# Kernel optimization log

Measured on AMD Instinct MI355X. Metric: run time of the kernel, lower is better.

Reference implementation:

```python
import jax, jax.numpy as jnp
import numpy as np


def setup_inputs() -> dict:
    key = jax.random.key(0)
    ks = jax.random.split(key, 16)
    B, S, D, H = 32, 2048, 512, 512
    s = 1.0 / np.sqrt(H)
    inp = {
        "x": jax.random.normal(ks[0], (B, H), jnp.float32),
        "context": jax.random.normal(ks[1], (B, S, D), jnp.float32),
        "mask": jnp.zeros((B, S), jnp.bool_),  # False = valid position
        "Wi": jax.random.normal(ks[2], (H, H), jnp.float32) * s,
        "bi": jax.random.normal(ks[3], (H,), jnp.float32) * s,
        "Wc0": jax.random.normal(ks[4], (H, D), jnp.float32) * s,
        "bc0": jax.random.normal(ks[5], (H,), jnp.float32) * s,
        "Wc1": jax.random.normal(ks[6], (H, D), jnp.float32) * s,
        "bc1": jax.random.normal(ks[7], (H,), jnp.float32) * s,
        "Wc2": jax.random.normal(ks[8], (H, D), jnp.float32) * s,
        "bc2": jax.random.normal(ks[9], (H,), jnp.float32) * s,
        "Wc3": jax.random.normal(ks[10], (H, D), jnp.float32) * s,
        "bc3": jax.random.normal(ks[11], (H,), jnp.float32) * s,
        "V": jax.random.uniform(ks[12], (H,), jnp.float32, -s, s),
    }
    return inp


def reference(x, context, mask, Wi, bi, Wc0, bc0, Wc1, bc1, Wc2, bc2, Wc3, bc3, V):
    # mask: True = masked out in the original API; module flips it first.
    valid = ~mask  # [B, S], True = keep

    inp = (x @ Wi.T + bi)[:, :, None]  # [B, H, 1]

    def proj(W, b):
        # Conv1d(D, H, kernel=1) on context.permute(0,2,1) == token-wise GEMM
        return jnp.einsum("bsd,hd->bhs", context, W) + b[None, :, None]  # [B, H, S]

    ctx = jnp.concatenate(
        [proj(Wc0, bc0), proj(Wc1, bc1), proj(Wc2, bc2), proj(Wc3, bc3)], axis=2
    )  # [B, H, 4S]

    t = jnp.tanh(inp + ctx)                      # [B, H, 4S]
    att = jnp.einsum("h,bhs->bs", V, t)          # bmm(V[B,1,H], t).squeeze(1)
    att = 10.0 * jnp.tanh(att)                   # [B, 4S]

    valid4 = jnp.tile(valid, (1, 4))             # mask.repeat(1, 4)
    att = jnp.where(valid4, att, -jnp.inf)
    # torch.no_grad() around the masked fill detaches the rest of the graph
    att = jax.lax.stop_gradient(att)

    ans = jax.nn.softmax(att, axis=1)            # [B, 4S]
    p = jnp.max(ans, axis=1)
    indices = jnp.argmax(ans, axis=1)
    return indices[:, None], p[:, None], mask
```

## Files before the change

### kernel.cpp

```cpp
#include <hip/hip_runtime.h>
#include <math.h>

typedef __bf16 bf16x8 __attribute__((ext_vector_type(8)));
typedef float f32x4 __attribute__((ext_vector_type(4)));
typedef short short8v __attribute__((ext_vector_type(8)));

#define MARGIN 0.01f
#define NCAND 32

#define WAITL  do { asm volatile("s_waitcnt lgkmcnt(0)" ::: "memory"); __builtin_amdgcn_sched_barrier(0); } while (0)
#define WAITV0 do { asm volatile("s_waitcnt vmcnt(0)" ::: "memory"); __builtin_amdgcn_sched_barrier(0); } while (0)
#define WAITV3 do { asm volatile("s_waitcnt vmcnt(3)" ::: "memory"); __builtin_amdgcn_sched_barrier(0); } while (0)
#define BARR   do { __builtin_amdgcn_s_barrier(); __builtin_amdgcn_sched_barrier(0); } while (0)

__device__ __forceinline__ unsigned short f2bf(float f) {
  unsigned u = __float_as_uint(f);
  u += 0x7fffu + ((u >> 16) & 1u);
  return (unsigned short)(u >> 16);
}
__device__ __forceinline__ float tanh_fast(float x) {
  float e = __builtin_amdgcn_exp2f(x * 2.885390081777927f);
  return 1.f - 2.f * __builtin_amdgcn_rcpf(e + 1.f);
}
__device__ __forceinline__ void gl_lds16(const void* g, void* l) {
  __builtin_amdgcn_global_load_lds(
      (const __attribute__((address_space(1))) unsigned int*)g,
      (__attribute__((address_space(3))) unsigned int*)l, 16, 0, 0);
}
__device__ __forceinline__ int cvt_pk_bf16(float lo, float hi) {
  int r;
  asm("v_cvt_pk_bf16_f32 %0, %1, %2" : "=v"(r) : "v"(lo), "v"(hi));
  return r;
}
__device__ __forceinline__ float dpp_row_reduce(float v) {
  int x;
  x = __builtin_amdgcn_update_dpp(0, __builtin_bit_cast(int, v), 0x118, 0xf, 0xf, true);
  v += __builtin_bit_cast(float, x);
  x = __builtin_amdgcn_update_dpp(0, __builtin_bit_cast(int, v), 0x114, 0xf, 0xf, true);
  v += __builtin_bit_cast(float, x);
  x = __builtin_amdgcn_update_dpp(0, __builtin_bit_cast(int, v), 0x112, 0xf, 0xf, true);
  v += __builtin_bit_cast(float, x);
  x = __builtin_amdgcn_update_dpp(0, __builtin_bit_cast(int, v), 0x111, 0xf, 0xf, true);
  v += __builtin_bit_cast(float, x);
  return v;
}

__global__ __launch_bounds__(256) void prep_small_k(
    const float* __restrict__ x, const float* __restrict__ Wi,
    const float* __restrict__ bi,
    const float* __restrict__ w0, const float* __restrict__ w1,
    const float* __restrict__ w2, const float* __restrict__ w3,
    short* __restrict__ Whi, float* __restrict__ inp) {
  int bid = blockIdx.x;
  if (bid < 512) {
    int gid = bid * 256 + threadIdx.x;
    int c = gid & 3, row = (gid >> 2) & 511, TK = gid >> 11;
    int TN = TK >> 4, KS = TK & 15;
    const float* w = (TN == 0) ? w0 : (TN == 1) ? w1 : (TN == 2) ? w2 : w3;
    const float* src = w + (size_t)row * 512 + KS * 32 + c * 8;
    float f[8];
    *(float4*)&f[0] = *(const float4*)(src);
    *(float4*)&f[4] = *(const float4*)(src + 4);
    short8v hv;
    #pragma unroll
    for (int i = 0; i < 8; ++i) hv[i] = (short)f2bf(f[i]);
    *(short8v*)(Whi + (size_t)gid * 8) = hv;
  } else {
    int gid = (bid - 512) * 256 + threadIdx.x;
    int b = gid >> 9, h = gid & 511;
    const float* xr = x + b * 512;
    const float* wr = Wi + h * 512;
    float acc = bi[h];
    #pragma unroll 4
    for (int k = 0; k < 512; k += 4) {
      float4 xv = *(const float4*)(xr + k);
      float4 wv = *(const float4*)(wr + k);
      acc += xv.x * wv.x + xv.y * wv.y + xv.z * wv.z + xv.w * wv.w;
    }
    inp[gid] = acc;
  }
}

__global__ __launch_bounds__(1024, 4) void gemm_att_k(
    const float* __restrict__ ctx, const short* __restrict__ Whi,
    const float* __restrict__ inp,
    const float* __restrict__ bc0, const float* __restrict__ bc1,
    const float* __restrict__ bc2, const float* __restrict__ bc3,
    const float* __restrict__ V, float* __restrict__ att) {
  __shared__ __align__(16) char smem[3][49152];

  const int t = threadIdx.x;
  int d = blockIdx.x + (blockIdx.y << 3);
  int work = (d & 7) * 256 + (d >> 3);
  int mt = work >> 2, nt = work & 3;
  int b = mt >> 4;
  const float* bc = (nt == 0) ? bc0 : (nt == 1) ? bc1 : (nt == 2) ? bc2 : bc3;

  const int ar = t >> 3, apos = t & 7;
  const int aq = apos ^ (ar & 7);
  const float* aSrc = ctx + ((size_t)mt * 128 + ar) * 512 + aq * 4;

  auto stageA = [&](int tile, int slot) {
    gl_lds16(aSrc + tile * 32, (float*)&smem[slot][0] + t * 4);
  };
  auto stageB = [&](int tile, int slot) {
    const short* gB = Whi + (((size_t)nt * 16 + tile) << 14) + t * 8;
    short* lB = (short*)&smem[slot][16384] + t * 8;
    gl_lds16(gB,        lB);
    gl_lds16(gB + 8192, lB + 8192);
  };

  f32x4 acc[4][4];
  #pragma unroll
  for (int i = 0; i < 4; ++i)
    #pragma unroll
    for (int j = 0; j < 4; ++j) acc[i][j] = (f32x4){0.f, 0.f, 0.f, 0.f};

  const int lane = t & 63, wid = t >> 6;
  const int wr = wid >> 3, wc = wid & 7;
  const int fr = lane & 15, fq = lane >> 4;
  const int s7 = fr & 7;
  const int p0 = (fq * 2) ^ s7;
  const int bbase = (wc * 64 + fr) * 32 + fq * 8;

  stageA(0, 0); stageB(0, 0);
  stageA(1, 1); stageB(1, 1);
  WAITV3;
  BARR;

  #pragma unroll
  for (int tt = 0; tt < 16; ++tt) {
    const int slot = tt % 3;
    const float* As = (const float*)&smem[slot][0];
    const short* Bs = (const short*)&smem[slot][16384];
    if (tt < 14) { stageA(tt + 2, (tt + 2) % 3); stageB(tt + 2, (tt + 2) % 3); }
    bf16x8 a[4], bv[4];
    #pragma unroll
    for (int mi = 0; mi < 4; ++mi) {
      int rowb = (wr * 64 + mi * 16 + fr) * 32;
      f32x4 c0 = *(const f32x4*)(As + rowb + p0 * 4);
      f32x4 c1 = *(const f32x4*)(As + rowb + (p0 ^ 1) * 4);
      int4 w;
      w.x = cvt_pk_bf16(c0[0], c0[1]);
      w.y = cvt_pk_bf16(c0[2], c0[3]);
      w.z = cvt_pk_bf16(c1[0], c1[1]);
      w.w = cvt_pk_bf16(c1[2], c1[3]);
      a[mi] = __builtin_bit_cast(bf16x8, w);
    }
    #pragma unroll
    for (int ni = 0; ni < 4; ++ni) bv[ni] = *(const bf16x8*)(Bs + bbase + ni * 512);
    WAITL;
    __builtin_amdgcn_s_setprio(1);
    #pragma unroll
    for (int mi = 0; mi < 4; ++mi)
      #pragma unroll
      for (int ni = 0; ni < 4; ++ni)
        acc[mi][ni] = __builtin_amdgcn_mfma_f32_16x16x32_bf16(a[mi], bv[ni], acc[mi][ni], 0, 0, 0);
    __builtin_amdgcn_s_setprio(0);
    __builtin_amdgcn_sched_barrier(0);
    if (tt < 14) { WAITV3; }
    else if (tt == 14) { WAITV0; }
    BARR;
  }

  float vV[4], vP[4];
  #pragma unroll
  for (int ni = 0; ni < 4; ++ni) {
    int j = wc * 64 + ni * 16 + fr;
    vV[ni] = V[j];
    vP[ni] = inp[b * 512 + j] + bc[j];
  }
  size_t abatt = (size_t)b * 8192 + (size_t)nt * 2048;
  #pragma unroll
  for (int mi = 0; mi < 4; ++mi) {
    #pragma unroll
    for (int r = 0; r < 4; ++r) {
      float sum = 0.f;
      #pragma unroll
      for (int ni = 0; ni < 4; ++ni)
        sum += vV[ni] * tanh_fast(vP[ni] + acc[mi][ni][r]);
      sum = dpp_row_reduce(sum);
      if (fr == 15) {
        int s2 = (mt & 15) * 128 + wr * 64 + mi * 16 + fq * 4 + r;
        atomicAdd(&att[abatt + s2], sum);
      }
    }
  }
}

__global__ __launch_bounds__(1024) void tail_k(const float* __restrict__ att,
    const unsigned char* __restrict__ mask, const float* __restrict__ ctx,
    const float* __restrict__ Wc0, const float* __restrict__ Wc1,
    const float* __restrict__ Wc2, const float* __restrict__ Wc3,
    const float* __restrict__ bc0, const float* __restrict__ bc1,
    const float* __restrict__ bc2, const float* __restrict__ bc3,
    const float* __restrict__ inp, const float* __restrict__ V,
    float* __restrict__ out) {
  int b = blockIdx.x, t = threadIdx.x;
  __shared__ float sred[1024];
  __shared__ float sctx[512];
  __shared__ int scnt;
  __shared__ int scand_j[NCAND];
  __shared__ float scand_a[NCAND];
  __shared__ float sexact[NCAND];

  if (t == 0) scnt = 0;
  float bm = -1e30f;
  for (int j = t; j < 8192; j += 1024) {
    if (mask[b * 2048 + (j & 2047)]) continue;
    bm = fmaxf(bm, att[(size_t)b * 8192 + j]);
  }
  sred[t] = bm;
  __syncthreads();
  for (int s2 = 512; s2 > 0; s2 >>= 1) {
    if (t < s2) sred[t] = fmaxf(sred[t], sred[t + s2]);
    __syncthreads();
  }
  float mx = sred[0];
  float Lref = 10.f * tanhf(mx);
  __syncthreads();
  float se = 0.f;
  for (int j = t; j < 8192; j += 1024) {
    if (mask[b * 2048 + (j & 2047)]) continue;
    float a = att[(size_t)b * 8192 + j];
    se += expf(10.f * tanhf(a) - Lref);
    if (a >= mx - MARGIN) {
      int slot = atomicAdd(&scnt, 1);
      if (slot < NCAND) { scand_j[slot] = j; scand_a[slot] = a; }
    }
  }
  sred[t] = se;
  __syncthreads();
  for (int s2 = 512; s2 > 0; s2 >>= 1) {
    if (t < s2) sred[t] += sred[t + s2];
    __syncthreads();
  }
  float den = sred[0];
  int n = min(scnt, NCAND);
  for (int j = t; j < 2048; j += 1024)
    out[64 + b * 2048 + j] = mask[b * 2048 + j] ? 1.0f : 0.0f;
  for (int i = 0; i < n; ++i) {
    int jj = scand_j[i];
    int g = jj >> 11, s = jj & 2047;
    const float* W  = (g == 0) ? Wc0 : (g == 1) ? Wc1 : (g == 2) ? Wc2 : Wc3;
    const float* bc = (g == 0) ? bc0 : (g == 1) ? bc1 : (g == 2) ? bc2 : bc3;
    const float* cr = ctx + ((size_t)b * 2048 + s) * 512;
    __syncthreads();
    if (t < 512) sctx[t] = cr[t];
    __syncthreads();
    float total = 0.f;
    if (t < 512) {
      const float* wrp = W + (size_t)t * 512;
      float acc = 0.f;
      #pragma unroll 4
      for (int k = 0; k < 512; k += 4) {
        float4 wv = *(const float4*)(wrp + k);
        acc += wv.x * sctx[k] + wv.y * sctx[k + 1] + wv.z * sctx[k + 2] + wv.w * sctx[k + 3];
      }
      total = V[t] * tanhf(inp[b * 512 + t] + bc[t] + acc);
    }
    sred[t] = total;
    __syncthreads();
    for (int s2 = 512; s2 > 0; s2 >>= 1) {
      if (t < s2) sred[t] += sred[t + s2];
      __syncthreads();
    }
    if (t == 0) sexact[i] = sred[0];
  }
  __syncthreads();
  if (t == 0) {
    float dd = den, best = -1e30f;
    int bj = 0x7fffffff;
    for (int i = 0; i < n; ++i) {
      float e = sexact[i];
      int j = scand_j[i];
      dd += expf(10.f * tanhf(e) - Lref) - expf(10.f * tanhf(scand_a[i]) - Lref);
      if (e > best || (e == best && j < bj)) { best = e; bj = j; }
    }
    out[b] = (float)bj;
    out[32 + b] = expf(10.f * tanhf(best) - Lref) / dd;
  }
}

extern "C" void kernel_launch(void* const* d_in, const int* in_sizes, int n_in,
                              void* d_out, int out_size, void* d_ws, size_t ws_size,
                              hipStream_t stream) {
  const float* x    = (const float*)d_in[0];
  const float* ctx  = (const float*)d_in[1];
  const unsigned char* mask = (const unsigned char*)d_in[2];
  const float* Wi   = (const float*)d_in[3];
  const float* bi   = (const float*)d_in[4];
  const float* Wc0  = (const float*)d_in[5];
  const float* bc0  = (const float*)d_in[6];
  const float* Wc1  = (const float*)d_in[7];
  const float* bc1  = (const float*)d_in[8];
  const float* Wc2  = (const float*)d_in[9];
  const float* bc2  = (const float*)d_in[10];
  const float* Wc3  = (const float*)d_in[11];
  const float* bc3  = (const float*)d_in[12];
  const float* V    = (const float*)d_in[13];
  float* out = (float*)d_out;

  float* inp = (float*)d_ws;
  float* att = inp + 16384;
  short* Whi = (short*)(att + 262144);

  hipMemsetAsync(att, 0, 262144 * sizeof(float), stream);
  prep_small_k<<<576, 256, 0, stream>>>(x, Wi, bi, Wc0, Wc1, Wc2, Wc3, Whi, inp);
  gemm_att_k<<<dim3(8, 256), 1024, 0, stream>>>(ctx, Whi,
      inp, bc0, bc1, bc2, bc3, V, att);
  tail_k<<<32, 1024, 0, stream>>>(att, mask, ctx, Wc0, Wc1, Wc2, Wc3,
      bc0, bc1, bc2, bc3, inp, V, out);
}
```

Measured before the change: 291.5 us.

## Convert context to bf16 once while staging into LDS and use fast exp/tanh

The A operand (context tile) is now loaded into registers, converted to bf16 once and written to LDS as bf16. Previously fp32 went straight to LDS through direct global->LDS loads and was converted per wave on every read. This halves A's LDS footprint and cuts the redundant conversions each wave performed. In exchange the loop waits for all vector loads (vmcnt(0)) each iteration before writing, which reduces overlap. The softmax kernel also replaces expf/tanhf with hardware exp2-based approximations.

```diff
diff --git a/kernel.cpp b/kernel.cpp
--- a/kernel.cpp
+++ b/kernel.cpp
@@ -10,7 +10,6 @@
 
 #define WAITL  do { asm volatile("s_waitcnt lgkmcnt(0)" ::: "memory"); __builtin_amdgcn_sched_barrier(0); } while (0)
 #define WAITV0 do { asm volatile("s_waitcnt vmcnt(0)" ::: "memory"); __builtin_amdgcn_sched_barrier(0); } while (0)
-#define WAITV3 do { asm volatile("s_waitcnt vmcnt(3)" ::: "memory"); __builtin_amdgcn_sched_barrier(0); } while (0)
 #define BARR   do { __builtin_amdgcn_s_barrier(); __builtin_amdgcn_sched_barrier(0); } while (0)
 
 __device__ __forceinline__ unsigned short f2bf(float f) {
@@ -21,6 +20,9 @@
 __device__ __forceinline__ float tanh_fast(float x) {
   float e = __builtin_amdgcn_exp2f(x * 2.885390081777927f);
   return 1.f - 2.f * __builtin_amdgcn_rcpf(e + 1.f);
+}
+__device__ __forceinline__ float exp_fast(float x) {
+  return __builtin_amdgcn_exp2f(x * 1.4426950408889634f);
 }
 __device__ __forceinline__ void gl_lds16(const void* g, void* l) {
   __builtin_amdgcn_global_load_lds(
@@ -87,7 +89,7 @@
     const float* __restrict__ bc0, const float* __restrict__ bc1,
     const float* __restrict__ bc2, const float* __restrict__ bc3,
     const float* __restrict__ V, float* __restrict__ att) {
-  __shared__ __align__(16) char smem[3][49152];
+  __shared__ __align__(16) char smem[3][40960];
 
   const int t = threadIdx.x;
   int d = blockIdx.x + (blockIdx.y << 3);
@@ -96,16 +98,21 @@
   int b = mt >> 4;
   const float* bc = (nt == 0) ? bc0 : (nt == 1) ? bc1 : (nt == 2) ? bc2 : bc3;
 
-  const int ar = t >> 3, apos = t & 7;
-  const int aq = apos ^ (ar & 7);
-  const float* aSrc = ctx + ((size_t)mt * 128 + ar) * 512 + aq * 4;
-
-  auto stageA = [&](int tile, int slot) {
-    gl_lds16(aSrc + tile * 32, (float*)&smem[slot][0] + t * 4);
+  const int ac = t >> 1, ah = t & 1;
+  const int ar = ac >> 2, aq = ac & 3;
+  const float* aSrc = ctx + ((size_t)mt * 128 + ar) * 512 + aq * 8 + ah * 4;
+  const int aDstOff = ar * 32 + aq * 8 + ah * 4;
+
+  auto loadA = [&](int tile) -> float4 { return *(const float4*)(aSrc + tile * 32); };
+  auto writeA = [&](const float4& v, int slot) {
+    int2 w;
+    w.x = cvt_pk_bf16(v.x, v.y);
+    w.y = cvt_pk_bf16(v.z, v.w);
+    *(int2*)((short*)&smem[slot][0] + aDstOff) = w;
   };
   auto stageB = [&](int tile, int slot) {
     const short* gB = Whi + (((size_t)nt * 16 + tile) << 14) + t * 8;
-    short* lB = (short*)&smem[slot][16384] + t * 8;
+    short* lB = (short*)&smem[slot][8192] + t * 8;
     gl_lds16(gB,        lB);
     gl_lds16(gB + 8192, lB + 8192);
   };
@@ -119,36 +126,29 @@
   const int lane = t & 63, wid = t >> 6;
   const int wr = wid >> 3, wc = wid & 7;
   const int fr = lane & 15, fq = lane >> 4;
-  const int s7 = fr & 7;
-  const int p0 = (fq * 2) ^ s7;
-  const int bbase = (wc * 64 + fr) * 32 + fq * 8;
-
-  stageA(0, 0); stageB(0, 0);
-  stageA(1, 1); stageB(1, 1);
-  WAITV3;
+  const int abase = (wr * 64 + fr) * 32 + fq * 8;
+  const int bbase = 8192 / 2 + (wc * 64 + fr) * 32 + fq * 8;
+
+  {
+    float4 a0 = loadA(0), a1 = loadA(1);
+    stageB(0, 0); stageB(1, 1);
+    WAITV0;
+    writeA(a0, 0); writeA(a1, 1);
+    WAITL;
+  }
   BARR;
 
   #pragma unroll
   for (int tt = 0; tt < 16; ++tt) {
     const int slot = tt % 3;
-    const float* As = (const float*)&smem[slot][0];
-    const short* Bs = (const short*)&smem[slot][16384];
-    if (tt < 14) { stageA(tt + 2, (tt + 2) % 3); stageB(tt + 2, (tt + 2) % 3); }
+    const short* As = (const short*)&smem[slot][0];
+    float4 anext;
+    if (tt < 14) { anext = loadA(tt + 2); stageB(tt + 2, (tt + 2) % 3); }
     bf16x8 a[4], bv[4];
     #pragma unroll
-    for (int mi = 0; mi < 4; ++mi) {
-      int rowb = (wr * 64 + mi * 16 + fr) * 32;
-      f32x4 c0 = *(const f32x4*)(As + rowb + p0 * 4);
-      f32x4 c1 = *(const f32x4*)(As + rowb + (p0 ^ 1) * 4);
-      int4 w;
-      w.x = cvt_pk_bf16(c0[0], c0[1]);
-      w.y = cvt_pk_bf16(c0[2], c0[3]);
-      w.z = cvt_pk_bf16(c1[0], c1[1]);
-      w.w = cvt_pk_bf16(c1[2], c1[3]);
-      a[mi] = __builtin_bit_cast(bf16x8, w);
-    }
-    #pragma unroll
-    for (int ni = 0; ni < 4; ++ni) bv[ni] = *(const bf16x8*)(Bs + bbase + ni * 512);
+    for (int mi = 0; mi < 4; ++mi) a[mi] = *(const bf16x8*)(As + abase + mi * 512);
+    #pragma unroll
+    for (int ni = 0; ni < 4; ++ni) bv[ni] = *(const bf16x8*)(As + bbase + ni * 512);
     WAITL;
     __builtin_amdgcn_s_setprio(1);
     #pragma unroll
@@ -158,8 +158,10 @@
         acc[mi][ni] = __builtin_amdgcn_mfma_f32_16x16x32_bf16(a[mi], bv[ni], acc[mi][ni], 0, 0, 0);
     __builtin_amdgcn_s_setprio(0);
     __builtin_amdgcn_sched_barrier(0);
-    if (tt < 14) { WAITV3; }
-    else if (tt == 14) { WAITV0; }
+    if (tt < 14) {
+      WAITV0;
+      writeA(anext, (tt + 2) % 3);
+    }
     BARR;
   }
 
@@ -217,13 +219,13 @@
     __syncthreads();
   }
   float mx = sred[0];
-  float Lref = 10.f * tanhf(mx);
+  float Lref = 10.f * tanh_fast(mx);
   __syncthreads();
   float se = 0.f;
   for (int j = t; j < 8192; j += 1024) {
     if (mask[b * 2048 + (j & 2047)]) continue;
     float a = att[(size_t)b * 8192 + j];
-    se += expf(10.f * tanhf(a) - Lref);
+    se += exp_fast(10.f * tanh_fast(a) - Lref);
     if (a >= mx - MARGIN) {
       int slot = atomicAdd(&scnt, 1);
       if (slot < NCAND) { scand_j[slot] = j; scand_a[slot] = a; }
@@ -274,11 +276,11 @@
     for (int i = 0; i < n; ++i) {
       float e = sexact[i];
       int j = scand_j[i];
-      dd += expf(10.f * tanhf(e) - Lref) - expf(10.f * tanhf(scand_a[i]) - Lref);
+      dd += exp_fast(10.f * tanh_fast(e) - Lref) - exp_fast(10.f * tanh_fast(scand_a[i]) - Lref);
       if (e > best || (e == best && j < bj)) { best = e; bj = j; }
     }
     out[b] = (float)bj;
-    out[32 + b] = expf(10.f * tanhf(best) - Lref) / dd;
+    out[32 + b] = exp_fast(10.f * tanh_fast(best) - Lref) / dd;
   }
 }
 
```

After: 268.4 us, median of 3. 1.09x faster.
